# Kernel tuning notes

Measured on AMD Instinct MI355X. Metric: run time of the kernel, lower is better.

The kernel has to match this reference:

```python
import jax, jax.numpy as jnp
import numpy as np

B, L = 64, 4096
NIN, NST = 8, 16
CIN = NIN + NST          # 24 input channels to FNO
WIDTH = 64               # hidden_channels
MODES = 32               # n_modes_height
NL = 4                   # n_layers
PROJ = 128               # projection hidden width (standard FNO1d)


def setup_inputs() -> dict:
    key = jax.random.key(0)
    ks = jax.random.split(key, 12)
    u = jax.random.normal(ks[0], (B, L, NIN), jnp.float32)
    z = jax.random.normal(ks[1], (B, NST), jnp.float32)
    t = jax.random.normal(ks[2], (B,), jnp.float32)
    # lifting
    fc0_w = jax.random.normal(ks[3], (CIN, WIDTH), jnp.float32) / np.sqrt(CIN)
    fc0_b = jnp.zeros((WIDTH,), jnp.float32)
    # spectral weights (real/imag parts) and 1x1 skip convs per layer
    scale = 1.0 / (WIDTH * WIDTH)
    spec_wr = scale * jax.random.normal(ks[4], (NL, WIDTH, WIDTH, MODES), jnp.float32)
    spec_wi = scale * jax.random.normal(ks[5], (NL, WIDTH, WIDTH, MODES), jnp.float32)
    skip_w = jax.random.normal(ks[6], (NL, WIDTH, WIDTH), jnp.float32) / np.sqrt(WIDTH)
    skip_b = jnp.zeros((NL, WIDTH), jnp.float32)
    # projection
    fc1_w = jax.random.normal(ks[7], (WIDTH, PROJ), jnp.float32) / np.sqrt(WIDTH)
    fc1_b = jnp.zeros((PROJ,), jnp.float32)
    fc2_w = jax.random.normal(ks[8], (PROJ, NST), jnp.float32) / np.sqrt(PROJ)
    fc2_b = jnp.zeros((NST,), jnp.float32)
    return dict(u=u, z=z, t=t, fc0_w=fc0_w, fc0_b=fc0_b,
                spec_wr=spec_wr, spec_wi=spec_wi, skip_w=skip_w, skip_b=skip_b,
                fc1_w=fc1_w, fc1_b=fc1_b, fc2_w=fc2_w, fc2_b=fc2_b)


def _fno_forward(x, fc0_w, fc0_b, spec_wr, spec_wi, skip_w, skip_b,
                 fc1_w, fc1_b, fc2_w, fc2_b):
    # x: [B, L, CIN]
    n = x.shape[1]
    h = jnp.einsum('blc,cw->blw', x, fc0_w) + fc0_b        # lift -> [B, L, W]
    h = jnp.transpose(h, (0, 2, 1))                         # [B, W, L] channels-first
    nfreq = n // 2 + 1
    for l in range(NL):
        hf = jnp.fft.rfft(h, axis=-1)                       # [B, W, nfreq] complex
        wc = (spec_wr[l] + 1j * spec_wi[l]).astype(hf.dtype)  # [W, W, M]
        of = jnp.einsum('bim,iom->bom', hf[..., :MODES], wc)  # truncated-mode matmul
        full = jnp.zeros(h.shape[:2] + (nfreq,), hf.dtype).at[..., :MODES].set(of)
        spec = jnp.fft.irfft(full, n=n, axis=-1)            # [B, W, L]
        skip = jnp.einsum('bil,io->bol', h, skip_w[l]) + skip_b[l][None, :, None]
        h = spec + skip
        if l < NL - 1:
            h = jax.nn.gelu(h)
    h = jnp.transpose(h, (0, 2, 1))                         # [B, L, W]
    q = jax.nn.gelu(jnp.einsum('blw,wp->blp', h, fc1_w) + fc1_b)
    return jnp.einsum('blp,po->blo', q, fc2_w) + fc2_b      # [B, L, NST]


def reference(u, z, t, fc0_w, fc0_b, spec_wr, spec_wi, skip_w, skip_b,
              fc1_w, fc1_b, fc2_w, fc2_b):
    # z.tile(seq_len).reshape(B, seq_len, n_state) == broadcast along time
    rep_z = jnp.broadcast_to(z[:, None, :], (z.shape[0], u.shape[1], z.shape[1]))
    x = jnp.concatenate([u, rep_z], axis=-1)                # [B, L, CIN]
    outs = _fno_forward(x, fc0_w, fc0_b, spec_wr, spec_wi, skip_w, skip_b,
                        fc1_w, fc1_b, fc2_w, fc2_b)         # [B, L, NST]
    return outs[:, -1, :]                                   # [B, NST]
```

## Files before the change

kernel.cpp:

```cpp
#include <hip/hip_runtime.h>
#include <math.h>

#define LL 4096
#define NB 64
#define WW 64
#define NMODES 32
#define NCIN 24
#define NLAY 4
#define NPROJ 128
#define NSTC 16
#define NSPLIT 16
#define PK 136

typedef __attribute__((ext_vector_type(8))) short short8;
typedef __attribute__((ext_vector_type(4))) float f32x4;

static __device__ __forceinline__ float gelu_tanh(float x){
    const float c0 = 0.7978845608028654f;
    const float c1 = 0.044715f;
    float t = tanhf(c0*(x + c1*x*x*x));
    return 0.5f*x*(1.0f+t);
}

static __device__ __forceinline__ unsigned short bf16_rn(float v){
    unsigned int u = __float_as_uint(v);
    unsigned int r = (u + 0x7fffu + ((u>>16)&1u)) >> 16;
    return (unsigned short)r;
}
static __device__ __forceinline__ float bf16f(unsigned short h){
    return __uint_as_float(((unsigned int)h)<<16);
}
static __device__ __forceinline__ void split_store(unsigned short* hi, unsigned short* lo,
                                                   size_t idx, float v){
    unsigned short h = bf16_rn(v);
    hi[idx] = h;
    lo[idx] = bf16_rn(v - bf16f(h));
}

__global__ void k_tables(unsigned short* __restrict__ TD_hi, unsigned short* __restrict__ TD_lo,
                         unsigned short* __restrict__ TI_hi, unsigned short* __restrict__ TI_lo){
    int idx = blockIdx.x*256 + threadIdx.x;
    if (idx >= LL*NMODES) return;
    int x = idx & (LL-1);
    int k = idx >> 12;
    int ph = (k*x) & (LL-1);
    float ang = (6.283185307179586f/(float)LL)*(float)ph;
    float c = cosf(ang), s = sinf(ang);
    split_store(TD_hi, TD_lo, (size_t)k*LL + x, c);
    split_store(TD_hi, TD_lo, (size_t)(k+NMODES)*LL + x, -s);
    float tc, ts;
    if (k == 0){ tc = 1.0f/(float)LL; ts = 0.0f; }
    else { tc = (2.0f/(float)LL)*c; ts = -(2.0f/(float)LL)*s; }
    split_store(TI_hi, TI_lo, (size_t)k*LL + x, tc);
    split_store(TI_hi, TI_lo, (size_t)(k+NMODES)*LL + x, ts);
}

__global__ void k_wt(const float* __restrict__ wr, const float* __restrict__ wi,
                     float* __restrict__ wrT, float* __restrict__ wiT,
                     const float* __restrict__ skw,
                     unsigned short* __restrict__ skwT_hi, unsigned short* __restrict__ skwT_lo){
    int idx = blockIdx.x*256 + threadIdx.x;
    if (idx < NLAY*WW*WW*NMODES){
        int m = idx & 31;
        int o = (idx >> 5) & 63;
        int i = (idx >> 11) & 63;
        int l = idx >> 17;
        size_t dst = (((size_t)l*NMODES + m)*WW + i)*WW + o;
        wrT[dst] = wr[idx];
        wiT[dst] = wi[idx];
    }
    if (idx < NLAY*WW*WW){
        int o = idx & 63;
        int i = (idx >> 6) & 63;
        int l = idx >> 12;
        float v = skw[((size_t)l*WW + i)*WW + o];
        split_store(skwT_hi, skwT_lo, ((size_t)l*WW + o)*WW + i, v);
    }
}

__global__ void k_lift(const float* __restrict__ u, const float* __restrict__ z,
                       const float* __restrict__ w0, const float* __restrict__ b0,
                       unsigned short* __restrict__ h_hi, unsigned short* __restrict__ h_lo){
    __shared__ float Ws[NCIN*WW];
    __shared__ float Bs[WW];
    __shared__ float Zs[16];
    int b = blockIdx.y;
    int x0 = blockIdx.x*256;
    int tid = threadIdx.x;
    for (int i = tid; i < NCIN*WW; i += 256) Ws[i] = w0[i];
    if (tid < WW) Bs[tid] = b0[tid];
    if (tid < 16) Zs[tid] = z[b*16 + tid];
    __syncthreads();
    int x = x0 + tid;
    const float4* up = (const float4*)(u + ((size_t)b*LL + x)*8);
    float4 a0 = up[0], a1 = up[1];
    float ur[8] = {a0.x,a0.y,a0.z,a0.w,a1.x,a1.y,a1.z,a1.w};
    float zr[16];
    #pragma unroll
    for (int j=0;j<16;j++) zr[j] = Zs[j];
    for (int c=0;c<WW;c++){
        float acc = Bs[c];
        #pragma unroll
        for (int j=0;j<8;j++)  acc += ur[j]*Ws[j*WW+c];
        #pragma unroll
        for (int j=0;j<16;j++) acc += zr[j]*Ws[(8+j)*WW+c];
        split_store(h_hi, h_lo, ((size_t)b*WW + c)*LL + x, acc);
    }
}

__global__ __launch_bounds__(256) void k_dft(
        const unsigned short* __restrict__ h_hi, const unsigned short* __restrict__ h_lo,
        const unsigned short* __restrict__ td_hi, const unsigned short* __restrict__ td_lo,
        float* __restrict__ part){
    int rt = blockIdx.x;
    int s  = blockIdx.y;
    int tid = threadIdx.x;
    int w = tid >> 6;
    int lane = tid & 63;
    int g = lane >> 4;
    int i = lane & 15;
    f32x4 acc[4];
    #pragma unroll
    for (int nf=0;nf<4;nf++) acc[nf] = (f32x4){0.f,0.f,0.f,0.f};
    size_t arow = (size_t)(rt*64 + w*16 + i)*LL;
    int xbase = s*256;
    for (int ks=0; ks<8; ks++){
        int xk = xbase + ks*32 + g*8;
        short8 a_hi = *(const short8*)(h_hi + arow + xk);
        short8 a_lo = *(const short8*)(h_lo + arow + xk);
        #pragma unroll
        for (int nf=0;nf<4;nf++){
            size_t brow = (size_t)(nf*16 + i)*LL + xk;
            short8 b_hi = *(const short8*)(td_hi + brow);
            short8 b_lo = *(const short8*)(td_lo + brow);
            acc[nf] = __builtin_amdgcn_mfma_f32_16x16x32_bf16(a_lo, b_hi, acc[nf], 0,0,0);
            acc[nf] = __builtin_amdgcn_mfma_f32_16x16x32_bf16(a_hi, b_lo, acc[nf], 0,0,0);
            acc[nf] = __builtin_amdgcn_mfma_f32_16x16x32_bf16(a_hi, b_hi, acc[nf], 0,0,0);
        }
    }
    int drow = rt*64 + w*16 + g*4;
    #pragma unroll
    for (int nf=0;nf<4;nf++)
        #pragma unroll
        for (int r=0;r<4;r++)
            part[((size_t)s*4096 + drow + r)*64 + nf*16 + i] = acc[nf][r];
}

__global__ void k_reduce(const float* __restrict__ part, float* __restrict__ hfT){
    int e = blockIdx.x*256 + threadIdx.x;
    int i    = e & 63;
    int reim = (e >> 6) & 1;
    int m    = (e >> 7) & 31;
    int b    = e >> 12;
    int n = m + 32*reim;
    size_t rowoff = ((size_t)b*WW + i)*64 + n;
    float s = 0.f;
    #pragma unroll
    for (int sp=0; sp<NSPLIT; sp++) s += part[(size_t)sp*262144 + rowoff];
    hfT[e] = s;
}

__global__ void k_mix(const float* __restrict__ hfT, const float* __restrict__ wrT,
                      const float* __restrict__ wiT, float* __restrict__ of,
                      unsigned short* __restrict__ of_hi, unsigned short* __restrict__ of_lo){
    int m = blockIdx.x, b = blockIdx.y;
    int o = threadIdx.x;
    __shared__ float hr[64], hi_[64];
    const float* row = hfT + ((size_t)b*NMODES + m)*128;
    hr[o] = row[o];
    hi_[o] = row[64+o];
    __syncthreads();
    float ar = 0.f, ai = 0.f;
    const float* wr = wrT + (size_t)m*4096;
    const float* wi = wiT + (size_t)m*4096;
    for (int i=0;i<64;i++){
        float wrv = wr[i*64+o], wiv = wi[i*64+o];
        float r = hr[i], im = hi_[i];
        ar += r*wrv - im*wiv;
        ai += r*wiv + im*wrv;
    }
    size_t base = ((size_t)b*WW+o)*64;
    of[base + m]      = ar;
    of[base + 32 + m] = ai;
    split_store(of_hi, of_lo, base + m, ar);
    split_store(of_hi, of_lo, base + 32 + m, ai);
}

__global__ __launch_bounds__(256) void k_fused(
        const unsigned short* __restrict__ h_hi, const unsigned short* __restrict__ h_lo,
        const unsigned short* __restrict__ ti_hi, const unsigned short* __restrict__ ti_lo,
        const unsigned short* __restrict__ skwT_hi, const unsigned short* __restrict__ skwT_lo,
        const unsigned short* __restrict__ of_hi, const unsigned short* __restrict__ of_lo,
        const float* __restrict__ skb,
        unsigned short* __restrict__ ho_hi, unsigned short* __restrict__ ho_lo){
    __shared__ __align__(16) char ldsraw[2*64*PK*2];
    unsigned short* Bs_hi = (unsigned short*)ldsraw;
    unsigned short* Bs_lo = Bs_hi + 64*PK;
    int b  = blockIdx.y;
    int X0 = blockIdx.x*64;
    int tid = threadIdx.x;
    int xl = tid & 63;
    int kq = tid >> 6;
    for (int pl=0; pl<2; pl++){
        const unsigned short* hsrc = pl ? h_lo : h_hi;
        const unsigned short* tsrc = pl ? ti_lo : ti_hi;
        unsigned short* Bs = pl ? Bs_lo : Bs_hi;
        #pragma unroll
        for (int it=0; it<8; it++){
            int k0 = (kq + it*4)*4;
            const unsigned short* s0 = (k0 < 64)
                ? (hsrc + ((size_t)(b*64 + k0))*LL + X0 + xl)
                : (tsrc + ((size_t)(k0-64))*LL + X0 + xl);
            unsigned short v0 = s0[0], v1 = s0[LL], v2 = s0[2*LL], v3 = s0[3*LL];
            unsigned long long pk = (unsigned long long)v0
                                  | ((unsigned long long)v1<<16)
                                  | ((unsigned long long)v2<<32)
                                  | ((unsigned long long)v3<<48);
            *(unsigned long long*)(Bs + xl*PK + k0) = pk;
        }
    }
    __syncthreads();
    int w = tid >> 6, lane = tid & 63, g = lane >> 4, j = lane & 15;
    f32x4 acc[4];
    #pragma unroll
    for (int mf=0; mf<4; mf++) acc[mf] = (f32x4){0.f,0.f,0.f,0.f};
    const unsigned short* BrH = Bs_hi + (w*16 + j)*PK;
    const unsigned short* BrL = Bs_lo + (w*16 + j)*PK;
    #pragma unroll
    for (int ks=0; ks<4; ks++){
        short8 bh = *(const short8*)(BrH + ks*32 + g*8);
        short8 bl = *(const short8*)(BrL + ks*32 + g*8);
        #pragma unroll
        for (int mf=0; mf<4; mf++){
            int o = mf*16 + j;
            const unsigned short *pa_hi, *pa_lo;
            if (ks < 2){
                pa_hi = skwT_hi + (o<<6) + ks*32 + g*8;
                pa_lo = skwT_lo + (o<<6) + ks*32 + g*8;
            } else {
                size_t bo = ((size_t)(b*64 + o))<<6;
                pa_hi = of_hi + bo + (ks-2)*32 + g*8;
                pa_lo = of_lo + bo + (ks-2)*32 + g*8;
            }
            short8 ah = *(const short8*)pa_hi;
            short8 al = *(const short8*)pa_lo;
            acc[mf] = __builtin_amdgcn_mfma_f32_16x16x32_bf16(al, bh, acc[mf], 0,0,0);
            acc[mf] = __builtin_amdgcn_mfma_f32_16x16x32_bf16(ah, bl, acc[mf], 0,0,0);
            acc[mf] = __builtin_amdgcn_mfma_f32_16x16x32_bf16(ah, bh, acc[mf], 0,0,0);
        }
    }
    __syncthreads();
    unsigned int* T = (unsigned int*)ldsraw;
    #pragma unroll
    for (int mf=0; mf<4; mf++){
        #pragma unroll
        for (int r=0; r<4; r++){
            int o = mf*16 + g*4 + r;
            float v = acc[mf][r] + skb[o];
            v = gelu_tanh(v);
            unsigned short h16 = bf16_rn(v);
            unsigned short l16 = bf16_rn(v - bf16f(h16));
            T[o*65 + w*16 + j] = (unsigned int)h16 | ((unsigned int)l16 << 16);
        }
    }
    __syncthreads();
    #pragma unroll
    for (int q=0; q<4; q++){
        int f = tid + q*256;
        int o = f >> 4, seg = f & 15;
        const unsigned int* tr = T + o*65 + seg*4;
        unsigned int t0=tr[0], t1=tr[1], t2=tr[2], t3=tr[3];
        unsigned long long hv = (unsigned long long)(t0 & 0xffffu)
            | ((unsigned long long)(t1 & 0xffffu)<<16)
            | ((unsigned long long)(t2 & 0xffffu)<<32)
            | ((unsigned long long)(t3 & 0xffffu)<<48);
        unsigned long long lv = (unsigned long long)(t0 >> 16)
            | ((unsigned long long)(t1 >> 16)<<16)
            | ((unsigned long long)(t2 >> 16)<<32)
            | ((unsigned long long)(t3 >> 16)<<48);
        size_t base = ((size_t)(b*64 + o))*LL + X0 + seg*4;
        *(unsigned long long*)(ho_hi + base) = hv;
        *(unsigned long long*)(ho_lo + base) = lv;
    }
}

__global__ void k_final(const unsigned short* __restrict__ h3_hi,
                        const unsigned short* __restrict__ h3_lo,
                        const float* __restrict__ of,
                        const float* __restrict__ skw, const float* __restrict__ skb,
                        const unsigned short* __restrict__ ti_hi,
                        const unsigned short* __restrict__ ti_lo,
                        const float* __restrict__ w1, const float* __restrict__ b1,
                        const float* __restrict__ w2, const float* __restrict__ b2,
                        float* __restrict__ out){
    int b = blockIdx.x;
    int tid = threadIdx.x;
    __shared__ float hch[64];
    __shared__ float til[64];
    __shared__ float hv[64];
    __shared__ float qv[128];
    if (tid < 64){
        size_t idx = ((size_t)(b*64 + tid))*LL + (LL-1);
        hch[tid] = bf16f(h3_hi[idx]) + bf16f(h3_lo[idx]);
    } else {
        size_t idx = (size_t)(tid-64)*LL + (LL-1);
        til[tid-64] = bf16f(ti_hi[idx]) + bf16f(ti_lo[idx]);
    }
    __syncthreads();
    if (tid < 64){
        int o = tid;
        float acc = skb[o];
        const float* ofr = of + ((size_t)b*WW + o)*64;
        #pragma unroll
        for (int j=0;j<64;j++) acc += ofr[j]*til[j];
        #pragma unroll
        for (int i=0;i<64;i++) acc += hch[i]*skw[i*64+o];
        hv[o] = acc;
    }
    __syncthreads();
    {
        int p = tid;
        float acc = b1[p];
        for (int o=0;o<64;o++) acc += hv[o]*w1[o*NPROJ+p];
        qv[p] = gelu_tanh(acc);
    }
    __syncthreads();
    if (tid < NSTC){
        int s = tid;
        float acc = b2[s];
        for (int p=0;p<NPROJ;p++) acc += qv[p]*w2[p*NSTC+s];
        out[b*NSTC + s] = acc;
    }
}

extern "C" void kernel_launch(void* const* d_in, const int* in_sizes, int n_in,
                              void* d_out, int out_size, void* d_ws, size_t ws_size,
                              hipStream_t stream) {
    const float* u     = (const float*)d_in[0];
    const float* z     = (const float*)d_in[1];
    const float* fc0w  = (const float*)d_in[3];
    const float* fc0b  = (const float*)d_in[4];
    const float* swr   = (const float*)d_in[5];
    const float* swi   = (const float*)d_in[6];
    const float* skw   = (const float*)d_in[7];
    const float* skb   = (const float*)d_in[8];
    const float* fc1w  = (const float*)d_in[9];
    const float* fc1b  = (const float*)d_in[10];
    const float* fc2w  = (const float*)d_in[11];
    const float* fc2b  = (const float*)d_in[12];
    float* out = (float*)d_out;

    const size_t SZ_HP   = (size_t)4096*LL*2;
    const size_t SZ_TBL  = (size_t)64*LL*2;
    const size_t SZ_HFT  = (size_t)64*32*128*4;
    const size_t SZ_OF   = (size_t)64*64*64*4;
    const size_t SZ_OFP  = (size_t)64*64*64*2;
    const size_t SZ_WT   = (size_t)NLAY*NMODES*WW*WW*4;
    const size_t SZ_SKT  = (size_t)NLAY*WW*WW*2;

    size_t need = 4*SZ_HP + 4*SZ_TBL + SZ_HFT + SZ_OF + 2*SZ_OFP + 2*SZ_WT + 2*SZ_SKT;
    if (ws_size < need) return;

    char* p = (char*)d_ws;
    unsigned short* hA_hi = (unsigned short*)p; p += SZ_HP;
    unsigned short* hA_lo = (unsigned short*)p; p += SZ_HP;
    unsigned short* hB_hi = (unsigned short*)p; p += SZ_HP;
    unsigned short* hB_lo = (unsigned short*)p; p += SZ_HP;
    unsigned short* TD_hi = (unsigned short*)p; p += SZ_TBL;
    unsigned short* TD_lo = (unsigned short*)p; p += SZ_TBL;
    unsigned short* TI_hi = (unsigned short*)p; p += SZ_TBL;
    unsigned short* TI_lo = (unsigned short*)p; p += SZ_TBL;
    float* hfT   = (float*)p; p += SZ_HFT;
    float* of    = (float*)p; p += SZ_OF;
    unsigned short* of_hi = (unsigned short*)p; p += SZ_OFP;
    unsigned short* of_lo = (unsigned short*)p; p += SZ_OFP;
    float* wrT   = (float*)p; p += SZ_WT;
    float* wiT   = (float*)p; p += SZ_WT;
    unsigned short* skwT_hi = (unsigned short*)p; p += SZ_SKT;
    unsigned short* skwT_lo = (unsigned short*)p; p += SZ_SKT;

    k_tables<<<(LL*NMODES+255)/256, 256, 0, stream>>>(TD_hi, TD_lo, TI_hi, TI_lo);
    k_wt<<<(NLAY*WW*WW*NMODES+255)/256, 256, 0, stream>>>(swr, swi, wrT, wiT,
                                                          skw, skwT_hi, skwT_lo);
    k_lift<<<dim3(LL/256, NB), 256, 0, stream>>>(u, z, fc0w, fc0b, hA_hi, hA_lo);

    unsigned short* cur_hi = hA_hi; unsigned short* cur_lo = hA_lo;
    unsigned short* nxt_hi = hB_hi; unsigned short* nxt_lo = hB_lo;
    for (int l = 0; l < NLAY; l++){
        float* part = (float*)nxt_hi;
        k_dft<<<dim3(64, NSPLIT), 256, 0, stream>>>(cur_hi, cur_lo, TD_hi, TD_lo, part);
        k_reduce<<<(64*32*128)/256, 256, 0, stream>>>(part, hfT);
        k_mix<<<dim3(NMODES, NB), 64, 0, stream>>>(hfT, wrT + (size_t)l*NMODES*WW*WW,
                                                   wiT + (size_t)l*NMODES*WW*WW,
                                                   of, of_hi, of_lo);
        if (l < NLAY-1){
            k_fused<<<dim3(LL/64, NB), 256, 0, stream>>>(cur_hi, cur_lo, TI_hi, TI_lo,
                skwT_hi + (size_t)l*WW*WW, skwT_lo + (size_t)l*WW*WW,
                of_hi, of_lo, skb + (size_t)l*WW, nxt_hi, nxt_lo);
            unsigned short* t;
            t = cur_hi; cur_hi = nxt_hi; nxt_hi = t;
            t = cur_lo; cur_lo = nxt_lo; nxt_lo = t;
        }
    }
    k_final<<<NB, 128, 0, stream>>>(cur_hi, cur_lo, of, skw + (size_t)3*WW*WW,
                                    skb + (size_t)3*WW, TI_hi, TI_lo,
                                    fc1w, fc1b, fc2w, fc2b, out);
}
```

Measured before the change: 657.1 us.

## Store activations channels-last to drop LDS staging in fused inverse-DFT kernel

Switches the hidden-state hi/lo bf16 buffers from [B,W,L] to [B,L,W] and the inverse-DFT table to x-major, so the fused skip+inverse-DFT kernel can load MFMA operands straight from global memory and write outputs without LDS transposes or barriers. The lift kernel now writes packed 4-channel chunks. The forward DFT kernel instead gathers its A operand with eight strided scalar loads per lane, which may cost more than the LDS work it replaces. GELU also switches from tanhf to an exp-based sigmoid form.

```diff
diff --git a/kernel.cpp b/kernel.cpp
--- a/kernel.cpp
+++ b/kernel.cpp
@@ -10,16 +10,15 @@
 #define NPROJ 128
 #define NSTC 16
 #define NSPLIT 16
-#define PK 136
 
 typedef __attribute__((ext_vector_type(8))) short short8;
 typedef __attribute__((ext_vector_type(4))) float f32x4;
 
-static __device__ __forceinline__ float gelu_tanh(float x){
+static __device__ __forceinline__ float gelu_fast(float x){
     const float c0 = 0.7978845608028654f;
     const float c1 = 0.044715f;
-    float t = tanhf(c0*(x + c1*x*x*x));
-    return 0.5f*x*(1.0f+t);
+    float u = c0*(x + c1*x*x*x);
+    return x / (1.0f + __expf(-2.0f*u));
 }
 
 static __device__ __forceinline__ unsigned short bf16_rn(float v){
@@ -38,7 +37,7 @@
 }
 
 __global__ void k_tables(unsigned short* __restrict__ TD_hi, unsigned short* __restrict__ TD_lo,
-                         unsigned short* __restrict__ TI_hi, unsigned short* __restrict__ TI_lo){
+                         unsigned short* __restrict__ TIk_hi, unsigned short* __restrict__ TIk_lo){
     int idx = blockIdx.x*256 + threadIdx.x;
     if (idx >= LL*NMODES) return;
     int x = idx & (LL-1);
@@ -51,8 +50,8 @@
     float tc, ts;
     if (k == 0){ tc = 1.0f/(float)LL; ts = 0.0f; }
     else { tc = (2.0f/(float)LL)*c; ts = -(2.0f/(float)LL)*s; }
-    split_store(TI_hi, TI_lo, (size_t)k*LL + x, tc);
-    split_store(TI_hi, TI_lo, (size_t)(k+NMODES)*LL + x, ts);
+    split_store(TIk_hi, TIk_lo, (size_t)x*64 + k, tc);
+    split_store(TIk_hi, TIk_lo, (size_t)x*64 + NMODES + k, ts);
 }
 
 __global__ void k_wt(const float* __restrict__ wr, const float* __restrict__ wi,
@@ -80,7 +79,7 @@
 
 __global__ void k_lift(const float* __restrict__ u, const float* __restrict__ z,
                        const float* __restrict__ w0, const float* __restrict__ b0,
-                       unsigned short* __restrict__ h_hi, unsigned short* __restrict__ h_lo){
+                       unsigned short* __restrict__ hT_hi, unsigned short* __restrict__ hT_lo){
     __shared__ float Ws[NCIN*WW];
     __shared__ float Bs[WW];
     __shared__ float Zs[16];
@@ -98,18 +97,29 @@
     float zr[16];
     #pragma unroll
     for (int j=0;j<16;j++) zr[j] = Zs[j];
-    for (int c=0;c<WW;c++){
-        float acc = Bs[c];
-        #pragma unroll
-        for (int j=0;j<8;j++)  acc += ur[j]*Ws[j*WW+c];
-        #pragma unroll
-        for (int j=0;j<16;j++) acc += zr[j]*Ws[(8+j)*WW+c];
-        split_store(h_hi, h_lo, ((size_t)b*WW + c)*LL + x, acc);
+    size_t rowbase = ((size_t)b*LL + x)*64;
+    for (int c0=0;c0<WW;c0+=4){
+        unsigned long long hv = 0ull, lv = 0ull;
+        #pragma unroll
+        for (int r=0;r<4;r++){
+            int c = c0 + r;
+            float acc = Bs[c];
+            #pragma unroll
+            for (int j=0;j<8;j++)  acc += ur[j]*Ws[j*WW+c];
+            #pragma unroll
+            for (int j=0;j<16;j++) acc += zr[j]*Ws[(8+j)*WW+c];
+            unsigned short h16 = bf16_rn(acc);
+            unsigned short l16 = bf16_rn(acc - bf16f(h16));
+            hv |= ((unsigned long long)h16) << (16*r);
+            lv |= ((unsigned long long)l16) << (16*r);
+        }
+        *(unsigned long long*)(hT_hi + rowbase + c0) = hv;
+        *(unsigned long long*)(hT_lo + rowbase + c0) = lv;
     }
 }
 
 __global__ __launch_bounds__(256) void k_dft(
-        const unsigned short* __restrict__ h_hi, const unsigned short* __restrict__ h_lo,
+        const unsigned short* __restrict__ hT_hi, const unsigned short* __restrict__ hT_lo,
         const unsigned short* __restrict__ td_hi, const unsigned short* __restrict__ td_lo,
         float* __restrict__ part){
     int rt = blockIdx.x;
@@ -122,12 +132,18 @@
     f32x4 acc[4];
     #pragma unroll
     for (int nf=0;nf<4;nf++) acc[nf] = (f32x4){0.f,0.f,0.f,0.f};
-    size_t arow = (size_t)(rt*64 + w*16 + i)*LL;
+    int ch = w*16 + i;
+    size_t bbase = (size_t)rt*LL;
     int xbase = s*256;
     for (int ks=0; ks<8; ks++){
         int xk = xbase + ks*32 + g*8;
-        short8 a_hi = *(const short8*)(h_hi + arow + xk);
-        short8 a_lo = *(const short8*)(h_lo + arow + xk);
+        short8 a_hi, a_lo;
+        size_t idx0 = (bbase + xk)*64 + ch;
+        #pragma unroll
+        for (int e=0;e<8;e++){
+            a_hi[e] = (short)hT_hi[idx0 + (size_t)e*64];
+            a_lo[e] = (short)hT_lo[idx0 + (size_t)e*64];
+        }
         #pragma unroll
         for (int nf=0;nf<4;nf++){
             size_t brow = (size_t)(nf*16 + i)*LL + xk;
@@ -187,60 +203,40 @@
 }
 
 __global__ __launch_bounds__(256) void k_fused(
-        const unsigned short* __restrict__ h_hi, const unsigned short* __restrict__ h_lo,
-        const unsigned short* __restrict__ ti_hi, const unsigned short* __restrict__ ti_lo,
+        const unsigned short* __restrict__ hT_hi, const unsigned short* __restrict__ hT_lo,
+        const unsigned short* __restrict__ tik_hi, const unsigned short* __restrict__ tik_lo,
         const unsigned short* __restrict__ skwT_hi, const unsigned short* __restrict__ skwT_lo,
         const unsigned short* __restrict__ of_hi, const unsigned short* __restrict__ of_lo,
         const float* __restrict__ skb,
-        unsigned short* __restrict__ ho_hi, unsigned short* __restrict__ ho_lo){
-    __shared__ __align__(16) char ldsraw[2*64*PK*2];
-    unsigned short* Bs_hi = (unsigned short*)ldsraw;
-    unsigned short* Bs_lo = Bs_hi + 64*PK;
+        unsigned short* __restrict__ hoT_hi, unsigned short* __restrict__ hoT_lo){
     int b  = blockIdx.y;
     int X0 = blockIdx.x*64;
     int tid = threadIdx.x;
-    int xl = tid & 63;
-    int kq = tid >> 6;
-    for (int pl=0; pl<2; pl++){
-        const unsigned short* hsrc = pl ? h_lo : h_hi;
-        const unsigned short* tsrc = pl ? ti_lo : ti_hi;
-        unsigned short* Bs = pl ? Bs_lo : Bs_hi;
-        #pragma unroll
-        for (int it=0; it<8; it++){
-            int k0 = (kq + it*4)*4;
-            const unsigned short* s0 = (k0 < 64)
-                ? (hsrc + ((size_t)(b*64 + k0))*LL + X0 + xl)
-                : (tsrc + ((size_t)(k0-64))*LL + X0 + xl);
-            unsigned short v0 = s0[0], v1 = s0[LL], v2 = s0[2*LL], v3 = s0[3*LL];
-            unsigned long long pk = (unsigned long long)v0
-                                  | ((unsigned long long)v1<<16)
-                                  | ((unsigned long long)v2<<32)
-                                  | ((unsigned long long)v3<<48);
-            *(unsigned long long*)(Bs + xl*PK + k0) = pk;
-        }
-    }
-    __syncthreads();
     int w = tid >> 6, lane = tid & 63, g = lane >> 4, j = lane & 15;
+    int xrow = X0 + w*16 + j;
+    size_t xb = ((size_t)b*LL + xrow)*64;
+    size_t tb = (size_t)xrow*64;
     f32x4 acc[4];
     #pragma unroll
     for (int mf=0; mf<4; mf++) acc[mf] = (f32x4){0.f,0.f,0.f,0.f};
-    const unsigned short* BrH = Bs_hi + (w*16 + j)*PK;
-    const unsigned short* BrL = Bs_lo + (w*16 + j)*PK;
     #pragma unroll
     for (int ks=0; ks<4; ks++){
-        short8 bh = *(const short8*)(BrH + ks*32 + g*8);
-        short8 bl = *(const short8*)(BrL + ks*32 + g*8);
+        int ko = ks*32 + g*8;
+        const unsigned short* bp_hi = (ks < 2) ? (hT_hi + xb + ko) : (tik_hi + tb + ko - 64);
+        const unsigned short* bp_lo = (ks < 2) ? (hT_lo + xb + ko) : (tik_lo + tb + ko - 64);
+        short8 bh = *(const short8*)bp_hi;
+        short8 bl = *(const short8*)bp_lo;
         #pragma unroll
         for (int mf=0; mf<4; mf++){
             int o = mf*16 + j;
             const unsigned short *pa_hi, *pa_lo;
             if (ks < 2){
-                pa_hi = skwT_hi + (o<<6) + ks*32 + g*8;
-                pa_lo = skwT_lo + (o<<6) + ks*32 + g*8;
+                pa_hi = skwT_hi + (o<<6) + ko;
+                pa_lo = skwT_lo + (o<<6) + ko;
             } else {
                 size_t bo = ((size_t)(b*64 + o))<<6;
-                pa_hi = of_hi + bo + (ks-2)*32 + g*8;
-                pa_lo = of_lo + bo + (ks-2)*32 + g*8;
+                pa_hi = of_hi + bo + ko - 64;
+                pa_lo = of_lo + bo + ko - 64;
             }
             short8 ah = *(const short8*)pa_hi;
             short8 al = *(const short8*)pa_lo;
@@ -249,47 +245,30 @@
             acc[mf] = __builtin_amdgcn_mfma_f32_16x16x32_bf16(ah, bh, acc[mf], 0,0,0);
         }
     }
-    __syncthreads();
-    unsigned int* T = (unsigned int*)ldsraw;
     #pragma unroll
     for (int mf=0; mf<4; mf++){
+        unsigned long long hv = 0ull, lv = 0ull;
         #pragma unroll
         for (int r=0; r<4; r++){
             int o = mf*16 + g*4 + r;
             float v = acc[mf][r] + skb[o];
-            v = gelu_tanh(v);
+            v = gelu_fast(v);
             unsigned short h16 = bf16_rn(v);
             unsigned short l16 = bf16_rn(v - bf16f(h16));
-            T[o*65 + w*16 + j] = (unsigned int)h16 | ((unsigned int)l16 << 16);
-        }
-    }
-    __syncthreads();
-    #pragma unroll
-    for (int q=0; q<4; q++){
-        int f = tid + q*256;
-        int o = f >> 4, seg = f & 15;
-        const unsigned int* tr = T + o*65 + seg*4;
-        unsigned int t0=tr[0], t1=tr[1], t2=tr[2], t3=tr[3];
-        unsigned long long hv = (unsigned long long)(t0 & 0xffffu)
-            | ((unsigned long long)(t1 & 0xffffu)<<16)
-            | ((unsigned long long)(t2 & 0xffffu)<<32)
-            | ((unsigned long long)(t3 & 0xffffu)<<48);
-        unsigned long long lv = (unsigned long long)(t0 >> 16)
-            | ((unsigned long long)(t1 >> 16)<<16)
-            | ((unsigned long long)(t2 >> 16)<<32)
-            | ((unsigned long long)(t3 >> 16)<<48);
-        size_t base = ((size_t)(b*64 + o))*LL + X0 + seg*4;
-        *(unsigned long long*)(ho_hi + base) = hv;
-        *(unsigned long long*)(ho_lo + base) = lv;
-    }
-}
-
-__global__ void k_final(const unsigned short* __restrict__ h3_hi,
-                        const unsigned short* __restrict__ h3_lo,
+            hv |= ((unsigned long long)h16) << (16*r);
+            lv |= ((unsigned long long)l16) << (16*r);
+        }
+        *(unsigned long long*)(hoT_hi + xb + mf*16 + g*4) = hv;
+        *(unsigned long long*)(hoT_lo + xb + mf*16 + g*4) = lv;
+    }
+}
+
+__global__ void k_final(const unsigned short* __restrict__ h3T_hi,
+                        const unsigned short* __restrict__ h3T_lo,
                         const float* __restrict__ of,
                         const float* __restrict__ skw, const float* __restrict__ skb,
-                        const unsigned short* __restrict__ ti_hi,
-                        const unsigned short* __restrict__ ti_lo,
+                        const unsigned short* __restrict__ tik_hi,
+                        const unsigned short* __restrict__ tik_lo,
                         const float* __restrict__ w1, const float* __restrict__ b1,
                         const float* __restrict__ w2, const float* __restrict__ b2,
                         float* __restrict__ out){
@@ -300,11 +279,11 @@
     __shared__ float hv[64];
     __shared__ float qv[128];
     if (tid < 64){
-        size_t idx = ((size_t)(b*64 + tid))*LL + (LL-1);
-        hch[tid] = bf16f(h3_hi[idx]) + bf16f(h3_lo[idx]);
+        size_t idx = ((size_t)b*LL + (LL-1))*64 + tid;
+        hch[tid] = bf16f(h3T_hi[idx]) + bf16f(h3T_lo[idx]);
     } else {
-        size_t idx = (size_t)(tid-64)*LL + (LL-1);
-        til[tid-64] = bf16f(ti_hi[idx]) + bf16f(ti_lo[idx]);
+        size_t idx = (size_t)(LL-1)*64 + (tid-64);
+        til[tid-64] = bf16f(tik_hi[idx]) + bf16f(tik_lo[idx]);
     }
     __syncthreads();
     if (tid < 64){
@@ -322,7 +301,7 @@
         int p = tid;
         float acc = b1[p];
         for (int o=0;o<64;o++) acc += hv[o]*w1[o*NPROJ+p];
-        qv[p] = gelu_tanh(acc);
+        qv[p] = gelu_fast(acc);
     }
     __syncthreads();
     if (tid < NSTC){
@@ -350,7 +329,7 @@
     const float* fc2b  = (const float*)d_in[12];
     float* out = (float*)d_out;
 
-    const size_t SZ_HP   = (size_t)4096*LL*2;
+    const size_t SZ_HP   = (size_t)NB*LL*64*2;
     const size_t SZ_TBL  = (size_t)64*LL*2;
     const size_t SZ_HFT  = (size_t)64*32*128*4;
     const size_t SZ_OF   = (size_t)64*64*64*4;
@@ -362,14 +341,14 @@
     if (ws_size < need) return;
 
     char* p = (char*)d_ws;
-    unsigned short* hA_hi = (unsigned short*)p; p += SZ_HP;
-    unsigned short* hA_lo = (unsigned short*)p; p += SZ_HP;
-    unsigned short* hB_hi = (unsigned short*)p; p += SZ_HP;
-    unsigned short* hB_lo = (unsigned short*)p; p += SZ_HP;
-    unsigned short* TD_hi = (unsigned short*)p; p += SZ_TBL;
-    unsigned short* TD_lo = (unsigned short*)p; p += SZ_TBL;
-    unsigned short* TI_hi = (unsigned short*)p; p += SZ_TBL;
-    unsigned short* TI_lo = (unsigned short*)p; p += SZ_TBL;
+    unsigned short* hAT_hi = (unsigned short*)p; p += SZ_HP;
+    unsigned short* hAT_lo = (unsigned short*)p; p += SZ_HP;
+    unsigned short* hBT_hi = (unsigned short*)p; p += SZ_HP;
+    unsigned short* hBT_lo = (unsigned short*)p; p += SZ_HP;
+    unsigned short* TD_hi  = (unsigned short*)p; p += SZ_TBL;
+    unsigned short* TD_lo  = (unsigned short*)p; p += SZ_TBL;
+    unsigned short* TIk_hi = (unsigned short*)p; p += SZ_TBL;
+    unsigned short* TIk_lo = (unsigned short*)p; p += SZ_TBL;
     float* hfT   = (float*)p; p += SZ_HFT;
     float* of    = (float*)p; p += SZ_OF;
     unsigned short* of_hi = (unsigned short*)p; p += SZ_OFP;
@@ -379,22 +358,22 @@
     unsigned short* skwT_hi = (unsigned short*)p; p += SZ_SKT;
     unsigned short* skwT_lo = (unsigned short*)p; p += SZ_SKT;
 
-    k_tables<<<(LL*NMODES+255)/256, 256, 0, stream>>>(TD_hi, TD_lo, TI_hi, TI_lo);
+    k_tables<<<(LL*NMODES+255)/256, 256, 0, stream>>>(TD_hi, TD_lo, TIk_hi, TIk_lo);
     k_wt<<<(NLAY*WW*WW*NMODES+255)/256, 256, 0, stream>>>(swr, swi, wrT, wiT,
                                                           skw, skwT_hi, skwT_lo);
-    k_lift<<<dim3(LL/256, NB), 256, 0, stream>>>(u, z, fc0w, fc0b, hA_hi, hA_lo);
-
-    unsigned short* cur_hi = hA_hi; unsigned short* cur_lo = hA_lo;
-    unsigned short* nxt_hi = hB_hi; unsigned short* nxt_lo = hB_lo;
+    k_lift<<<dim3(LL/256, NB), 256, 0, stream>>>(u, z, fc0w, fc0b, hAT_hi, hAT_lo);
+
+    unsigned short* cur_hi = hAT_hi; unsigned short* cur_lo = hAT_lo;
+    unsigned short* nxt_hi = hBT_hi; unsigned short* nxt_lo = hBT_lo;
     for (int l = 0; l < NLAY; l++){
         float* part = (float*)nxt_hi;
-        k_dft<<<dim3(64, NSPLIT), 256, 0, stream>>>(cur_hi, cur_lo, TD_hi, TD_lo, part);
+        k_dft<<<dim3(NB, NSPLIT), 256, 0, stream>>>(cur_hi, cur_lo, TD_hi, TD_lo, part);
         k_reduce<<<(64*32*128)/256, 256, 0, stream>>>(part, hfT);
         k_mix<<<dim3(NMODES, NB), 64, 0, stream>>>(hfT, wrT + (size_t)l*NMODES*WW*WW,
                                                    wiT + (size_t)l*NMODES*WW*WW,
                                                    of, of_hi, of_lo);
         if (l < NLAY-1){
-            k_fused<<<dim3(LL/64, NB), 256, 0, stream>>>(cur_hi, cur_lo, TI_hi, TI_lo,
+            k_fused<<<dim3(LL/64, NB), 256, 0, stream>>>(cur_hi, cur_lo, TIk_hi, TIk_lo,
                 skwT_hi + (size_t)l*WW*WW, skwT_lo + (size_t)l*WW*WW,
                 of_hi, of_lo, skb + (size_t)l*WW, nxt_hi, nxt_lo);
             unsigned short* t;
@@ -403,6 +382,6 @@
         }
     }
     k_final<<<NB, 128, 0, stream>>>(cur_hi, cur_lo, of, skw + (size_t)3*WW*WW,
-                                    skb + (size_t)3*WW, TI_hi, TI_lo,
+                                    skb + (size_t)3*WW, TIk_hi, TIk_lo,
                                     fc1w, fc1b, fc2w, fc2b, out);
 }
```

New measurement: 720.2 us. +9.6%, slower.
